# Performance work log

Measured on AMD Instinct MI355X. Metric: run time of the kernel, lower is better.

Reference implementation:

```python
import jax, jax.numpy as jnp
import numpy as np


def _conv1x1(x, W, b):
    # x: [B,C,H,W], W: [O,C], b: [O]  -> [B,O,H,W]
    return jnp.einsum('bchw,oc->bohw', x, W) + b[None, :, None, None]


def setup_inputs() -> dict:
    key = jax.random.key(0)
    ks = jax.random.split(key, 8)
    B, C, H, W = 16, 512, 48, 48
    d = C // 8
    scale = 0.02
    return {
        'feat_map': jax.random.normal(ks[0], (B, C, H, W), dtype=jnp.float32),
        'Wq': jax.random.normal(ks[1], (d, C), dtype=jnp.float32) * scale,
        'bq': jax.random.normal(ks[2], (d,), dtype=jnp.float32) * scale,
        'Wk': jax.random.normal(ks[3], (d, C), dtype=jnp.float32) * scale,
        'bk': jax.random.normal(ks[4], (d,), dtype=jnp.float32) * scale,
        'Wv': jax.random.normal(ks[5], (C, C), dtype=jnp.float32) * scale,
        'bv': jax.random.normal(ks[6], (C,), dtype=jnp.float32) * scale,
        'gamma': jnp.ones((1,), dtype=jnp.float32),
    }


def reference(feat_map, Wq, bq, Wk, bk, Wv, bv, gamma):
    # SAModule (DANet spatial attention):
    #   q = conv1(x) -> [B, d, HW] -> permute [B, HW, d]
    #   k = conv2(x) -> [B, d, HW]
    #   attn = softmax(q @ k, axis=-1)            # [B, HW, HW]
    #   v = conv3(x) -> [B, C, HW]
    #   out = v @ attn^T -> [B, C, H, W]
    #   y = gamma * out + x
    B, C, H, W = feat_map.shape
    HW = H * W
    q = _conv1x1(feat_map, Wq, bq).reshape(B, -1, HW).transpose(0, 2, 1)  # [B,HW,d]
    k = _conv1x1(feat_map, Wk, bk).reshape(B, -1, HW)                     # [B,d,HW]
    attn = jax.nn.softmax(jnp.einsum('bnd,bdm->bnm', q, k), axis=-1)      # [B,HW,HW]
    v = _conv1x1(feat_map, Wv, bv).reshape(B, C, HW)                      # [B,C,HW]
    out = jnp.einsum('bcm,bnm->bcn', v, attn).reshape(B, C, H, W)
    return gamma * out + feat_map
```

## Files before the change

kernel.cpp:

```cpp
#include <hip/hip_runtime.h>

typedef __bf16 bf16x8 __attribute__((ext_vector_type(8)));
typedef __bf16 bf16x4 __attribute__((ext_vector_type(4)));
typedef float  f32x4  __attribute__((ext_vector_type(4)));

constexpr int kHW = 2304;
constexpr int kC  = 512;

#if __has_builtin(__builtin_amdgcn_exp2f)
#define EXP2(x) __builtin_amdgcn_exp2f(x)
#else
#define EXP2(x) exp2f(x)
#endif

__device__ __forceinline__ void dma16(const __bf16* g, __bf16* l) {
    __builtin_amdgcn_global_load_lds(
        (const volatile __attribute__((address_space(1))) void*)g,
        (volatile __attribute__((address_space(3))) void*)l, 16, 0, 0);
}

__global__ void pack_weights(const float* __restrict__ Wq, const float* __restrict__ Wk,
                             const float* __restrict__ Wv, __bf16* __restrict__ Wqk2,
                             __bf16* __restrict__ Wvb2) {
    int idx = blockIdx.x * 256 + threadIdx.x;
    int o = idx >> 9, k = idx & 511, kb = k >> 6, kr = k & 63;
    if (idx < 64 * 512) {
        Wqk2[((size_t)kb * 128 + o) * 72 + kr]      = (__bf16)Wq[idx];
        Wqk2[((size_t)kb * 128 + 64 + o) * 72 + kr] = (__bf16)Wk[idx];
    }
    if (idx < 512 * 512)
        Wvb2[((size_t)kb * 512 + o) * 72 + kr] = (__bf16)Wv[idx];
}

__global__ void pack_x(const float* __restrict__ x, __bf16* __restrict__ XT2) {
    __shared__ __bf16 tile[64][65];
    int n0 = blockIdx.x * 64, kblk = blockIdx.y, b = blockIdx.z;
    int c0 = kblk * 64;
    int t = threadIdx.x;
    const float* xb = x + (size_t)b * kC * kHW;
#pragma unroll
    for (int rep = 0; rep < 16; ++rep) {
        int c_loc = rep * 4 + (t >> 6);
        int n_loc = t & 63;
        tile[c_loc][n_loc] = (__bf16)xb[(size_t)(c0 + c_loc) * kHW + n0 + n_loc];
    }
    __syncthreads();
    __bf16* dst = XT2 + ((size_t)b * 8 + kblk) * kHW * 72;
#pragma unroll
    for (int rep = 0; rep < 2; ++rep) {
        int item = rep * 256 + t;
        int n_loc = item >> 3, chunk = item & 7;
        bf16x8 v;
#pragma unroll
        for (int j = 0; j < 8; ++j) v[j] = tile[chunk * 8 + j][n_loc];
        *(bf16x8*)(dst + (size_t)(n0 + n_loc) * 72 + chunk * 8) = v;
    }
}

__global__ __launch_bounds__(256) void qkv_gemm(const __bf16* __restrict__ XT2,
                                                const __bf16* __restrict__ Wqk2,
                                                const __bf16* __restrict__ Wvb2,
                                                const float* __restrict__ bq,
                                                const float* __restrict__ bk,
                                                const float* __restrict__ bv,
                                                __bf16* __restrict__ qbuf,
                                                __bf16* __restrict__ kbuf,
                                                __bf16* __restrict__ vbuf2) {
    __shared__ __align__(16) __bf16 A_lds[128 * 72];
    __shared__ __align__(16) __bf16 B_lds[128 * 72];
    int bid = blockIdx.x;
    int work = (bid & 7) * 180 + (bid >> 3);
    int type = work % 5;
    int g = work / 5;
    int r0 = (g % 18) * 128;
    int b = g / 18;
    int t = threadIdx.x, wave = t >> 6, lane = t & 63, quad = lane >> 4, l16 = lane & 15;

    f32x4 acc[8][2];
#pragma unroll
    for (int i = 0; i < 8; ++i)
#pragma unroll
        for (int j = 0; j < 2; ++j) acc[i][j] = (f32x4){0.f, 0.f, 0.f, 0.f};

    for (int kb = 0; kb < 8; ++kb) {
        const __bf16* Asrc;
        const __bf16* Bsrc;
        if (type == 0) {
            Asrc = XT2 + (((size_t)b * 8 + kb) * kHW + r0) * 72;
            Bsrc = Wqk2 + (size_t)kb * 128 * 72;
        } else {
            Asrc = Wvb2 + ((size_t)kb * 512 + (type - 1) * 128) * 72;
            Bsrc = XT2 + (((size_t)b * 8 + kb) * kHW + r0) * 72;
        }
        __syncthreads();
        for (int ch = wave; ch < 18; ch += 4) {
            dma16(Asrc + ch * 512 + lane * 8, &A_lds[ch * 512]);
            dma16(Bsrc + ch * 512 + lane * 8, &B_lds[ch * 512]);
        }
        __syncthreads();
#pragma unroll
        for (int dk = 0; dk < 2; ++dk) {
            bf16x8 bfr[2];
#pragma unroll
            for (int ct = 0; ct < 2; ++ct)
                bfr[ct] = *(const bf16x8*)(&B_lds[(wave * 32 + ct * 16 + l16) * 72 + dk * 32 + quad * 8]);
#pragma unroll
            for (int rt = 0; rt < 8; ++rt) {
                bf16x8 a = *(const bf16x8*)(&A_lds[(rt * 16 + l16) * 72 + dk * 32 + quad * 8]);
#pragma unroll
                for (int ct = 0; ct < 2; ++ct)
                    acc[rt][ct] = __builtin_amdgcn_mfma_f32_16x16x32_bf16(a, bfr[ct], acc[rt][ct], 0, 0, 0);
            }
        }
    }

    if (type == 0) {
        constexpr float kLog2e = 1.4426950408889634f;
#pragma unroll
        for (int ct = 0; ct < 2; ++ct) {
            int o = wave * 32 + ct * 16 + l16;
            float bias = (o < 64) ? bq[o] : bk[o - 64];
            float scale = (o < 64) ? kLog2e : 1.0f;
#pragma unroll
            for (int rt = 0; rt < 8; ++rt)
#pragma unroll
                for (int r = 0; r < 4; ++r) {
                    int n = r0 + rt * 16 + quad * 4 + r;
                    __bf16 val = (__bf16)((acc[rt][ct][r] + bias) * scale);
                    if (o < 64) {
                        qbuf[((size_t)b * kHW + n) * 64 + o] = val;
                    } else {
                        int d = o - 64;
                        int dsw = (((d >> 3) ^ (n & 7)) << 3) | (d & 7);
                        kbuf[(((size_t)b * 72 + (n >> 5)) * 32 + (n & 31)) * 64 + dsw] = val;
                    }
                }
        }
    } else {
#pragma unroll
        for (int rt = 0; rt < 8; ++rt)
#pragma unroll
            for (int r = 0; r < 4; ++r) {
                int c = (type - 1) * 128 + rt * 16 + quad * 4 + r;
                float bias = bv[c];
#pragma unroll
                for (int ct = 0; ct < 2; ++ct) {
                    int m = r0 + wave * 32 + ct * 16 + l16;
                    vbuf2[(((size_t)b * 72 + (m >> 5)) * 512 + c) * 40 + (m & 31)] = (__bf16)(acc[rt][ct][r] + bias);
                }
            }
    }
}

__global__ __launch_bounds__(256, 4) void attn_kernel(const __bf16* __restrict__ qbuf,
                                                      const __bf16* __restrict__ kbuf,
                                                      const __bf16* __restrict__ vbuf2,
                                                      const float* __restrict__ x,
                                                      const float* __restrict__ gamma,
                                                      float* __restrict__ out) {
    __shared__ __align__(16) __bf16 K_lds[2][32 * 64];
    __shared__ __align__(16) __bf16 V_lds[2][128 * 40];
    __shared__ __align__(16) __bf16 P_lds[128 * 40];
    __shared__ float rs_lds[128];

    int bid = blockIdx.x;
    int work = (bid & 7) * 144 + (bid >> 3);
    int n0 = (work % 18) * 128;
    int pair = work / 18;
    int c0 = (pair & 3) * 128;
    int b = pair >> 2;
    int t = threadIdx.x, wave = t >> 6, lane = t & 63, quad = lane >> 4, l16 = lane & 15;
    const __bf16* q_b    = qbuf + (size_t)b * kHW * 64;
    const __bf16* k_base = kbuf + (size_t)b * 72 * 32 * 64;

    bf16x8 aq[2][2];
#pragma unroll
    for (int rt2 = 0; rt2 < 2; ++rt2)
#pragma unroll
        for (int dk = 0; dk < 2; ++dk)
            aq[rt2][dk] = *(const bf16x8*)(q_b + (size_t)(n0 + wave * 32 + rt2 * 16 + l16) * 64 + dk * 32 + quad * 8);

    f32x4 acc[2][8];
#pragma unroll
    for (int i = 0; i < 2; ++i)
#pragma unroll
        for (int j = 0; j < 8; ++j) acc[i][j] = (f32x4){0.f, 0.f, 0.f, 0.f};
    float rsum[2] = {0.f, 0.f};
    bf16x8 pf[2];

    auto issue_K = [&](int i, int buf) {
        const __bf16* ks = k_base + (size_t)i * 32 * 64;
        dma16(ks + wave * 512 + lane * 8, &K_lds[buf][wave * 512]);
    };
    auto issue_V = [&](int i, int buf) {
        const __bf16* vs = vbuf2 + (((size_t)b * 72 + i) * 512 + c0) * 40;
        for (int ch = wave; ch < 10; ch += 4)
            dma16(vs + ch * 512 + lane * 8, &V_lds[buf][ch * 512]);
    };
    auto qk_phase = [&](int j) {
        int kb_ = j & 1;
        __bf16* prow = &P_lds[(wave * 32 + l16) * 40 + quad * 4];
#pragma unroll
        for (int mt = 0; mt < 2; ++mt) {
            int row = mt * 16 + l16;
            int sw = (row & 7) << 3;
            bf16x8 kf0 = *(const bf16x8*)(&K_lds[kb_][row * 64 + ((quad * 8) ^ sw)]);
            bf16x8 kf1 = *(const bf16x8*)(&K_lds[kb_][row * 64 + ((32 + quad * 8) ^ sw)]);
#pragma unroll
            for (int rt2 = 0; rt2 < 2; ++rt2) {
                f32x4 s = (f32x4){0.f, 0.f, 0.f, 0.f};
                s = __builtin_amdgcn_mfma_f32_16x16x32_bf16(kf0, aq[rt2][0], s, 0, 0, 0);
                s = __builtin_amdgcn_mfma_f32_16x16x32_bf16(kf1, aq[rt2][1], s, 0, 0, 0);
                bf16x4 pv;
                float part = 0.f;
#pragma unroll
                for (int r = 0; r < 4; ++r) {
                    float e = EXP2(s[r]);
                    pv[r] = (__bf16)e;
                    part += e;
                }
                rsum[rt2] += part;
                *(bf16x4*)(prow + rt2 * 16 * 40 + mt * 16) = pv;
            }
        }
        pf[0] = *(const bf16x8*)(&P_lds[(wave * 32 + l16) * 40 + quad * 8]);
        pf[1] = *(const bf16x8*)(&P_lds[(wave * 32 + 16 + l16) * 40 + quad * 8]);
    };

    issue_K(0, 0);
    issue_V(0, 0);
    issue_K(1, 1);
    __syncthreads();
    qk_phase(0);

    for (int i = 0; i < 72; ++i) {
        __syncthreads();
        if (i + 2 < 72) issue_K(i + 2, i & 1);
        if (i + 1 < 72) issue_V(i + 1, (i + 1) & 1);

        __builtin_amdgcn_s_setprio(1);
#pragma unroll
        for (int ct = 0; ct < 8; ++ct) {
            bf16x8 vf = *(const bf16x8*)(&V_lds[i & 1][(ct * 16 + l16) * 40 + quad * 8]);
            acc[0][ct] = __builtin_amdgcn_mfma_f32_16x16x32_bf16(pf[0], vf, acc[0][ct], 0, 0, 0);
            acc[1][ct] = __builtin_amdgcn_mfma_f32_16x16x32_bf16(pf[1], vf, acc[1][ct], 0, 0, 0);
        }
        __builtin_amdgcn_s_setprio(0);

        if (i + 1 < 72) qk_phase(i + 1);
    }

#pragma unroll
    for (int rt2 = 0; rt2 < 2; ++rt2) {
        float v = rsum[rt2];
        v += __shfl_xor(v, 16);
        v += __shfl_xor(v, 32);
        if (quad == 0) rs_lds[wave * 32 + rt2 * 16 + l16] = v;
    }
    __syncthreads();

    float g = gamma[0];
    const float* x_b = x + (size_t)b * kC * kHW;
    float* out_b = out + (size_t)b * kC * kHW;
#pragma unroll
    for (int rt2 = 0; rt2 < 2; ++rt2) {
        float inv[4];
#pragma unroll
        for (int r = 0; r < 4; ++r) inv[r] = 1.f / rs_lds[wave * 32 + rt2 * 16 + quad * 4 + r];
#pragma unroll
        for (int ct = 0; ct < 8; ++ct) {
            int c = c0 + ct * 16 + l16;
            size_t base = (size_t)c * kHW + n0 + wave * 32 + rt2 * 16 + quad * 4;
            f32x4 xin = *(const f32x4*)(x_b + base);
            f32x4 y;
#pragma unroll
            for (int r = 0; r < 4; ++r) y[r] = g * acc[rt2][ct][r] * inv[r] + xin[r];
            *(f32x4*)(out_b + base) = y;
        }
    }
}

extern "C" void kernel_launch(void* const* d_in, const int* in_sizes, int n_in,
                              void* d_out, int out_size, void* d_ws, size_t ws_size,
                              hipStream_t stream) {
    const float* x     = (const float*)d_in[0];
    const float* Wq    = (const float*)d_in[1];
    const float* bq    = (const float*)d_in[2];
    const float* Wk    = (const float*)d_in[3];
    const float* bk    = (const float*)d_in[4];
    const float* Wv    = (const float*)d_in[5];
    const float* bv    = (const float*)d_in[6];
    const float* gamma = (const float*)d_in[7];
    float* out = (float*)d_out;

    char* ws = (char*)d_ws;
    __bf16* XT2   = (__bf16*)(ws);
    __bf16* Wqk2  = (__bf16*)(ws + 42467328);
    __bf16* Wvb2  = (__bf16*)(ws + 42614784);
    __bf16* qbuf  = (__bf16*)(ws + 43204608);
    __bf16* kbuf  = (__bf16*)(ws + 47923200);
    __bf16* vbuf2 = (__bf16*)(ws + 52641792);

    hipLaunchKernelGGL(pack_weights, dim3(1024), dim3(256), 0, stream, Wq, Wk, Wv, Wqk2, Wvb2);
    hipLaunchKernelGGL(pack_x, dim3(36, 8, 16), dim3(256), 0, stream, x, XT2);
    hipLaunchKernelGGL(qkv_gemm, dim3(1440), dim3(256), 0, stream,
                       XT2, Wqk2, Wvb2, bq, bk, bv, qbuf, kbuf, vbuf2);
    hipLaunchKernelGGL(attn_kernel, dim3(1152), dim3(256), 0, stream,
                       qbuf, kbuf, vbuf2, x, gamma, out);
}
```

Baseline: 374.5 us.

## Double-buffer QKV GEMM with XOR-swizzled 32-wide K panels

Repacks X and the weights into unpadded 32-element K panels whose 8-element slots are XOR-swizzled by row, replacing the 72-element padded rows used to avoid LDS bank conflicts. The QKV GEMM now double-buffers LDS and issues the async DMA for the next K slice before computing the current one, so each step needs one barrier instead of two and loads overlap with MFMA work. This also shrinks workspace and packed-data traffic. In exchange the K loop runs twice as many iterations with smaller tiles, and the qkv_gemm stage is a small share of total time next to the attention kernel.

```diff
diff --git a/kernel.cpp b/kernel.cpp
--- a/kernel.cpp
+++ b/kernel.cpp
@@ -19,20 +19,23 @@
         (volatile __attribute__((address_space(3))) void*)l, 16, 0, 0);
 }
 
+
 __global__ void pack_weights(const float* __restrict__ Wq, const float* __restrict__ Wk,
-                             const float* __restrict__ Wv, __bf16* __restrict__ Wqk2,
-                             __bf16* __restrict__ Wvb2) {
+                             const float* __restrict__ Wv, __bf16* __restrict__ Wqk2h,
+                             __bf16* __restrict__ Wvb2h) {
     int idx = blockIdx.x * 256 + threadIdx.x;
-    int o = idx >> 9, k = idx & 511, kb = k >> 6, kr = k & 63;
+    int o = idx >> 9, k = idx & 511;
+    int kb2 = k >> 5, slot = (k & 31) >> 3, j = k & 7;
+    int sl = (slot ^ (o & 3)) << 3;
     if (idx < 64 * 512) {
-        Wqk2[((size_t)kb * 128 + o) * 72 + kr]      = (__bf16)Wq[idx];
-        Wqk2[((size_t)kb * 128 + 64 + o) * 72 + kr] = (__bf16)Wk[idx];
+        Wqk2h[((size_t)kb2 * 128 + o) * 32 + sl + j]        = (__bf16)Wq[idx];
+        Wqk2h[((size_t)kb2 * 128 + 64 + o) * 32 + sl + j]   = (__bf16)Wk[idx];
     }
     if (idx < 512 * 512)
-        Wvb2[((size_t)kb * 512 + o) * 72 + kr] = (__bf16)Wv[idx];
-}
-
-__global__ void pack_x(const float* __restrict__ x, __bf16* __restrict__ XT2) {
+        Wvb2h[((size_t)kb2 * 512 + o) * 32 + sl + j] = (__bf16)Wv[idx];
+}
+
+__global__ void pack_x(const float* __restrict__ x, __bf16* __restrict__ XT2h) {
     __shared__ __bf16 tile[64][65];
     int n0 = blockIdx.x * 64, kblk = blockIdx.y, b = blockIdx.z;
     int c0 = kblk * 64;
@@ -45,7 +48,6 @@
         tile[c_loc][n_loc] = (__bf16)xb[(size_t)(c0 + c_loc) * kHW + n0 + n_loc];
     }
     __syncthreads();
-    __bf16* dst = XT2 + ((size_t)b * 8 + kblk) * kHW * 72;
 #pragma unroll
     for (int rep = 0; rep < 2; ++rep) {
         int item = rep * 256 + t;
@@ -53,21 +55,26 @@
         bf16x8 v;
 #pragma unroll
         for (int j = 0; j < 8; ++j) v[j] = tile[chunk * 8 + j][n_loc];
-        *(bf16x8*)(dst + (size_t)(n0 + n_loc) * 72 + chunk * 8) = v;
-    }
-}
-
-__global__ __launch_bounds__(256) void qkv_gemm(const __bf16* __restrict__ XT2,
-                                                const __bf16* __restrict__ Wqk2,
-                                                const __bf16* __restrict__ Wvb2,
+        int h = chunk >> 2;
+        int slot = chunk & 3;
+        int sl = (slot ^ (n_loc & 3)) << 3;
+        __bf16* dst = XT2h + (((size_t)b * 16 + kblk * 2 + h) * kHW + (n0 + n_loc)) * 32 + sl;
+        *(bf16x4*)(dst)     = (bf16x4){v[0], v[1], v[2], v[3]};
+        *(bf16x4*)(dst + 4) = (bf16x4){v[4], v[5], v[6], v[7]};
+    }
+}
+
+__global__ __launch_bounds__(256) void qkv_gemm(const __bf16* __restrict__ XT2h,
+                                                const __bf16* __restrict__ Wqk2h,
+                                                const __bf16* __restrict__ Wvb2h,
                                                 const float* __restrict__ bq,
                                                 const float* __restrict__ bk,
                                                 const float* __restrict__ bv,
                                                 __bf16* __restrict__ qbuf,
                                                 __bf16* __restrict__ kbuf,
                                                 __bf16* __restrict__ vbuf2) {
-    __shared__ __align__(16) __bf16 A_lds[128 * 72];
-    __shared__ __align__(16) __bf16 B_lds[128 * 72];
+    __shared__ __align__(16) __bf16 A_lds[2][128 * 32];
+    __shared__ __align__(16) __bf16 B_lds[2][128 * 32];
     int bid = blockIdx.x;
     int work = (bid & 7) * 180 + (bid >> 3);
     int type = work % 5;
@@ -75,6 +82,7 @@
     int r0 = (g % 18) * 128;
     int b = g / 18;
     int t = threadIdx.x, wave = t >> 6, lane = t & 63, quad = lane >> 4, l16 = lane & 15;
+    int slot8 = ((quad ^ (l16 & 3)) << 3);
 
     f32x4 acc[8][2];
 #pragma unroll
@@ -82,35 +90,37 @@
 #pragma unroll
         for (int j = 0; j < 2; ++j) acc[i][j] = (f32x4){0.f, 0.f, 0.f, 0.f};
 
-    for (int kb = 0; kb < 8; ++kb) {
+    auto stage = [&](int kb2, int buf) {
         const __bf16* Asrc;
         const __bf16* Bsrc;
         if (type == 0) {
-            Asrc = XT2 + (((size_t)b * 8 + kb) * kHW + r0) * 72;
-            Bsrc = Wqk2 + (size_t)kb * 128 * 72;
+            Asrc = XT2h + (((size_t)b * 16 + kb2) * kHW + r0) * 32;
+            Bsrc = Wqk2h + (size_t)kb2 * 128 * 32;
         } else {
-            Asrc = Wvb2 + ((size_t)kb * 512 + (type - 1) * 128) * 72;
-            Bsrc = XT2 + (((size_t)b * 8 + kb) * kHW + r0) * 72;
-        }
+            Asrc = Wvb2h + ((size_t)kb2 * 512 + (type - 1) * 128) * 32;
+            Bsrc = XT2h + (((size_t)b * 16 + kb2) * kHW + r0) * 32;
+        }
+        for (int ch = wave; ch < 8; ch += 4) {
+            dma16(Asrc + ch * 512 + lane * 8, &A_lds[buf][ch * 512]);
+            dma16(Bsrc + ch * 512 + lane * 8, &B_lds[buf][ch * 512]);
+        }
+    };
+
+    stage(0, 0);
+    for (int kb2 = 0; kb2 < 16; ++kb2) {
+        int buf = kb2 & 1;
         __syncthreads();
-        for (int ch = wave; ch < 18; ch += 4) {
-            dma16(Asrc + ch * 512 + lane * 8, &A_lds[ch * 512]);
-            dma16(Bsrc + ch * 512 + lane * 8, &B_lds[ch * 512]);
-        }
-        __syncthreads();
-#pragma unroll
-        for (int dk = 0; dk < 2; ++dk) {
-            bf16x8 bfr[2];
+        if (kb2 + 1 < 16) stage(kb2 + 1, buf ^ 1);
+        bf16x8 bfr[2];
+#pragma unroll
+        for (int ct = 0; ct < 2; ++ct)
+            bfr[ct] = *(const bf16x8*)(&B_lds[buf][(wave * 32 + ct * 16 + l16) * 32 + slot8]);
+#pragma unroll
+        for (int rt = 0; rt < 8; ++rt) {
+            bf16x8 a = *(const bf16x8*)(&A_lds[buf][(rt * 16 + l16) * 32 + slot8]);
 #pragma unroll
             for (int ct = 0; ct < 2; ++ct)
-                bfr[ct] = *(const bf16x8*)(&B_lds[(wave * 32 + ct * 16 + l16) * 72 + dk * 32 + quad * 8]);
-#pragma unroll
-            for (int rt = 0; rt < 8; ++rt) {
-                bf16x8 a = *(const bf16x8*)(&A_lds[(rt * 16 + l16) * 72 + dk * 32 + quad * 8]);
-#pragma unroll
-                for (int ct = 0; ct < 2; ++ct)
-                    acc[rt][ct] = __builtin_amdgcn_mfma_f32_16x16x32_bf16(a, bfr[ct], acc[rt][ct], 0, 0, 0);
-            }
+                acc[rt][ct] = __builtin_amdgcn_mfma_f32_16x16x32_bf16(a, bfr[ct], acc[rt][ct], 0, 0, 0);
         }
     }
 
@@ -294,17 +304,17 @@
     float* out = (float*)d_out;
 
     char* ws = (char*)d_ws;
-    __bf16* XT2   = (__bf16*)(ws);
-    __bf16* Wqk2  = (__bf16*)(ws + 42467328);
-    __bf16* Wvb2  = (__bf16*)(ws + 42614784);
-    __bf16* qbuf  = (__bf16*)(ws + 43204608);
-    __bf16* kbuf  = (__bf16*)(ws + 47923200);
-    __bf16* vbuf2 = (__bf16*)(ws + 52641792);
-
-    hipLaunchKernelGGL(pack_weights, dim3(1024), dim3(256), 0, stream, Wq, Wk, Wv, Wqk2, Wvb2);
-    hipLaunchKernelGGL(pack_x, dim3(36, 8, 16), dim3(256), 0, stream, x, XT2);
+    __bf16* XT2h  = (__bf16*)(ws);
+    __bf16* Wqk2h = (__bf16*)(ws + 37748736);
+    __bf16* Wvb2h = (__bf16*)(ws + 37879808);
+    __bf16* qbuf  = (__bf16*)(ws + 38404096);
+    __bf16* kbuf  = (__bf16*)(ws + 43122688);
+    __bf16* vbuf2 = (__bf16*)(ws + 47841280);
+
+    hipLaunchKernelGGL(pack_weights, dim3(1024), dim3(256), 0, stream, Wq, Wk, Wv, Wqk2h, Wvb2h);
+    hipLaunchKernelGGL(pack_x, dim3(36, 8, 16), dim3(256), 0, stream, x, XT2h);
     hipLaunchKernelGGL(qkv_gemm, dim3(1440), dim3(256), 0, stream,
-                       XT2, Wqk2, Wvb2, bq, bk, bv, qbuf, kbuf, vbuf2);
+                       XT2h, Wqk2h, Wvb2h, bq, bk, bv, qbuf, kbuf, vbuf2);
     hipLaunchKernelGGL(attn_kernel, dim3(1152), dim3(256), 0, stream,
                        qbuf, kbuf, vbuf2, x, gamma, out);
 }
```

Result: no change. 378.0 us (+0.9%).
